# Kernel optimization log

Measured on AMD Instinct MI355X. Metric: run time of the kernel, lower is better.

The kernel has to match this reference:

```python
import jax, jax.numpy as jnp
import numpy as np

IN_FEATURES = 4096
OUT_FEATURES = 4096
BATCH = 16384


def setup_inputs() -> dict:
    key = jax.random.key(0)
    k_x, k_w, k_b = jax.random.split(key, 3)
    x = jax.random.normal(k_x, (BATCH, IN_FEATURES), dtype=jnp.float32)
    # nn.Linear default init: U(-1/sqrt(in), 1/sqrt(in))
    bound = 1.0 / np.sqrt(IN_FEATURES)
    W = jax.random.uniform(k_w, (OUT_FEATURES, IN_FEATURES), dtype=jnp.float32,
                           minval=-bound, maxval=bound)
    bias = jax.random.uniform(k_b, (OUT_FEATURES,), dtype=jnp.float32,
                              minval=-bound, maxval=bound)
    return {"x": x, "W": W, "bias": bias}


def reference(x, W, bias):
    # Algebraic reduction: sum_j (x @ W.T + b)[i, j]
    #   = x @ sum_j W[j, :] + sum_j b[j]
    weight_sums = jnp.sum(W, axis=0)          # [in_features]
    bias_sum = jnp.sum(bias)                  # scalar
    out = x @ weight_sums + bias_sum          # [batch]
    return out[:, None]                       # [batch, 1]
```

## Files before the change

### kernel.cpp

```cpp
#include <hip/hip_runtime.h>

#define IN_F 4096
#define OUT_F 4096
#define BATCH 16384

#define NCHUNK 64
#define ROWS_PER_CHUNK (OUT_F / NCHUNK)
#define PART_F4 (IN_F / 4)
#define CS_OFF   (NCHUNK * IN_F)
#define BIAS_OFF (CS_OFF + IN_F)

__global__ __launch_bounds__(256) void colsum_part(
    const float* __restrict__ W, float* __restrict__ ws) {
  int col4 = blockIdx.x * 256 + threadIdx.x;
  int row0 = blockIdx.y * ROWS_PER_CHUNK;
  const float4* W4 = (const float4*)W;

  float4 acc = make_float4(0.f, 0.f, 0.f, 0.f);
  #pragma unroll 8
  for (int r = 0; r < ROWS_PER_CHUNK; ++r) {
    float4 v = W4[(size_t)(row0 + r) * PART_F4 + col4];
    acc.x += v.x; acc.y += v.y; acc.z += v.z; acc.w += v.w;
  }
  ((float4*)ws)[(size_t)blockIdx.y * PART_F4 + col4] = acc;
}

__global__ __launch_bounds__(256) void colsum_reduce(
    const float* __restrict__ bias, float* __restrict__ ws) {
  if (blockIdx.x < 4) {
    int col4 = blockIdx.x * 256 + threadIdx.x;
    const float4* p4 = (const float4*)ws;
    float4 acc = make_float4(0.f, 0.f, 0.f, 0.f);
    #pragma unroll 8
    for (int k = 0; k < NCHUNK; ++k) {
      float4 v = p4[(size_t)k * PART_F4 + col4];
      acc.x += v.x; acc.y += v.y; acc.z += v.z; acc.w += v.w;
    }
    ((float4*)(ws + CS_OFF))[col4] = acc;
  } else if (threadIdx.x < 64) {
    float b = 0.f;
    #pragma unroll
    for (int i = 0; i < OUT_F / 64; ++i) b += bias[threadIdx.x + i * 64];
    #pragma unroll
    for (int off = 32; off > 0; off >>= 1) b += __shfl_down(b, off);
    if (threadIdx.x == 0) ws[BIAS_OFF] = b;
  }
}

__global__ __launch_bounds__(256) void rowdot_kernel(
    const float* __restrict__ x, const float* __restrict__ ws,
    float* __restrict__ out) {
  int wave = threadIdx.x >> 6;
  int lane = threadIdx.x & 63;
  int row  = blockIdx.x * 4 + wave;

  const float4* xr  = (const float4*)(x + (size_t)row * IN_F);
  const float4* cs4 = (const float4*)(ws + CS_OFF);

  float acc = 0.f;
  #pragma unroll
  for (int it = 0; it < IN_F / 4 / 64; ++it) {
    float4 xv = xr[it * 64 + lane];
    float4 wv = cs4[it * 64 + lane];
    acc += xv.x * wv.x + xv.y * wv.y + xv.z * wv.z + xv.w * wv.w;
  }
  #pragma unroll
  for (int off = 32; off > 0; off >>= 1) acc += __shfl_down(acc, off);
  if (lane == 0) out[row] = acc + ws[BIAS_OFF];
}

extern "C" void kernel_launch(void* const* d_in, const int* in_sizes, int n_in,
                              void* d_out, int out_size, void* d_ws, size_t ws_size,
                              hipStream_t stream) {
  const float* x    = (const float*)d_in[0];
  const float* W    = (const float*)d_in[1];
  const float* bias = (const float*)d_in[2];
  float* out = (float*)d_out;
  float* ws  = (float*)d_ws;

  colsum_part<<<dim3(4, NCHUNK), 256, 0, stream>>>(W, ws);
  colsum_reduce<<<5, 256, 0, stream>>>(bias, ws);
  rowdot_kernel<<<BATCH / 4, 256, 0, stream>>>(x, ws, out);
}
```

Measured before the change: 395.9 us.

## Fuse column-sum, reduce and row-dot into one cooperative persistent kernel

Replaces the three launches with a single cooperative kernel of 1024 blocks that uses grid-wide syncs between the partial column-sum, final reduction and GEMV phases. The partial column sums now use 256 chunks so the W read is spread over more blocks, and the final weight vector is staged in shared memory for the row dot products. This removes kernel launch gaps and the tail idle time of the tiny reduce kernel. In exchange it adds two grid barriers, doubles the partial-sum workspace traffic, and depends on all 1024 blocks being co-resident, with a three-kernel fallback if the cooperative launch fails.

```diff
diff --git a/kernel.cpp b/kernel.cpp
--- a/kernel.cpp
+++ b/kernel.cpp
@@ -1,42 +1,113 @@
 #include <hip/hip_runtime.h>
+#include <hip/hip_cooperative_groups.h>
+
+namespace cg = cooperative_groups;
 
 #define IN_F 4096
 #define OUT_F 4096
 #define BATCH 16384
 
-#define NCHUNK 64
+#define NBLK 1024
+#define NCHUNK 256
 #define ROWS_PER_CHUNK (OUT_F / NCHUNK)
-#define PART_F4 (IN_F / 4)
 #define CS_OFF   (NCHUNK * IN_F)
 #define BIAS_OFF (CS_OFF + IN_F)
 
+__global__ __launch_bounds__(256, 4) void fused_kernel(
+    const float* __restrict__ x, const float* __restrict__ W,
+    const float* __restrict__ bias, float* __restrict__ ws,
+    float* __restrict__ out) {
+  cg::grid_group grid = cg::this_grid();
+  const int tid = threadIdx.x;
+  const int bid = blockIdx.x;
+
+  {
+    int colgroup = bid & 3;
+    int chunk    = bid >> 2;
+    int col4     = colgroup * 256 + tid;
+    int row0     = chunk * ROWS_PER_CHUNK;
+    const float4* W4 = (const float4*)W;
+    float4 acc = make_float4(0.f, 0.f, 0.f, 0.f);
+    #pragma unroll
+    for (int r = 0; r < ROWS_PER_CHUNK; ++r) {
+      float4 v = W4[(size_t)(row0 + r) * (IN_F / 4) + col4];
+      acc.x += v.x; acc.y += v.y; acc.z += v.z; acc.w += v.w;
+    }
+    ((float4*)ws)[(size_t)chunk * (IN_F / 4) + col4] = acc;
+  }
+
+  grid.sync();
+
+  if (bid < 16) {
+    int c = bid * 256 + tid;
+    float s = 0.f;
+    #pragma unroll 8
+    for (int k = 0; k < NCHUNK; ++k) s += ws[(size_t)k * IN_F + c];
+    ws[CS_OFF + c] = s;
+  } else if (bid == 16 && tid < 64) {
+    float b = 0.f;
+    #pragma unroll
+    for (int i = 0; i < OUT_F / 64; ++i) b += bias[tid + i * 64];
+    #pragma unroll
+    for (int off = 32; off > 0; off >>= 1) b += __shfl_down(b, off);
+    if (tid == 0) ws[BIAS_OFF] = b;
+  }
+
+  grid.sync();
+
+  __shared__ float4 sw[IN_F / 4];
+  __shared__ float sbias;
+  {
+    const float4* cs4 = (const float4*)(ws + CS_OFF);
+    #pragma unroll
+    for (int i = 0; i < 4; ++i) sw[tid + i * 256] = cs4[tid + i * 256];
+    if (tid == 0) sbias = ws[BIAS_OFF];
+  }
+  __syncthreads();
+
+  int wave = tid >> 6;
+  int lane = tid & 63;
+  #pragma unroll
+  for (int r = 0; r < 4; ++r) {
+    int row = bid * 16 + r * 4 + wave;
+    const float4* xr = (const float4*)(x + (size_t)row * IN_F);
+    float acc = 0.f;
+    #pragma unroll
+    for (int it = 0; it < 16; ++it) {
+      float4 xv = xr[it * 64 + lane];
+      float4 wv = sw[it * 64 + lane];
+      acc += xv.x * wv.x + xv.y * wv.y + xv.z * wv.z + xv.w * wv.w;
+    }
+    #pragma unroll
+    for (int off = 32; off > 0; off >>= 1) acc += __shfl_down(acc, off);
+    if (lane == 0) out[row] = acc + sbias;
+  }
+}
+
 __global__ __launch_bounds__(256) void colsum_part(
     const float* __restrict__ W, float* __restrict__ ws) {
-  int col4 = blockIdx.x * 256 + threadIdx.x;
-  int row0 = blockIdx.y * ROWS_PER_CHUNK;
+  int colgroup = blockIdx.x & 3;
+  int chunk    = blockIdx.x >> 2;
+  int col4     = colgroup * 256 + threadIdx.x;
+  int row0     = chunk * ROWS_PER_CHUNK;
   const float4* W4 = (const float4*)W;
-
   float4 acc = make_float4(0.f, 0.f, 0.f, 0.f);
-  #pragma unroll 8
+  #pragma unroll
   for (int r = 0; r < ROWS_PER_CHUNK; ++r) {
-    float4 v = W4[(size_t)(row0 + r) * PART_F4 + col4];
+    float4 v = W4[(size_t)(row0 + r) * (IN_F / 4) + col4];
     acc.x += v.x; acc.y += v.y; acc.z += v.z; acc.w += v.w;
   }
-  ((float4*)ws)[(size_t)blockIdx.y * PART_F4 + col4] = acc;
+  ((float4*)ws)[(size_t)chunk * (IN_F / 4) + col4] = acc;
 }
 
 __global__ __launch_bounds__(256) void colsum_reduce(
     const float* __restrict__ bias, float* __restrict__ ws) {
-  if (blockIdx.x < 4) {
-    int col4 = blockIdx.x * 256 + threadIdx.x;
-    const float4* p4 = (const float4*)ws;
-    float4 acc = make_float4(0.f, 0.f, 0.f, 0.f);
+  if (blockIdx.x < 16) {
+    int c = blockIdx.x * 256 + threadIdx.x;
+    float s = 0.f;
     #pragma unroll 8
-    for (int k = 0; k < NCHUNK; ++k) {
-      float4 v = p4[(size_t)k * PART_F4 + col4];
-      acc.x += v.x; acc.y += v.y; acc.z += v.z; acc.w += v.w;
-    }
-    ((float4*)(ws + CS_OFF))[col4] = acc;
+    for (int k = 0; k < NCHUNK; ++k) s += ws[(size_t)k * IN_F + c];
+    ws[CS_OFF + c] = s;
   } else if (threadIdx.x < 64) {
     float b = 0.f;
     #pragma unroll
@@ -53,13 +124,11 @@
   int wave = threadIdx.x >> 6;
   int lane = threadIdx.x & 63;
   int row  = blockIdx.x * 4 + wave;
-
   const float4* xr  = (const float4*)(x + (size_t)row * IN_F);
   const float4* cs4 = (const float4*)(ws + CS_OFF);
-
   float acc = 0.f;
   #pragma unroll
-  for (int it = 0; it < IN_F / 4 / 64; ++it) {
+  for (int it = 0; it < 16; ++it) {
     float4 xv = xr[it * 64 + lane];
     float4 wv = cs4[it * 64 + lane];
     acc += xv.x * wv.x + xv.y * wv.y + xv.z * wv.z + xv.w * wv.w;
@@ -78,7 +147,13 @@
   float* out = (float*)d_out;
   float* ws  = (float*)d_ws;
 
-  colsum_part<<<dim3(4, NCHUNK), 256, 0, stream>>>(W, ws);
-  colsum_reduce<<<5, 256, 0, stream>>>(bias, ws);
-  rowdot_kernel<<<BATCH / 4, 256, 0, stream>>>(x, ws, out);
+  void* args[] = {(void*)&x, (void*)&W, (void*)&bias, (void*)&ws, (void*)&out};
+  hipError_t err = hipLaunchCooperativeKernel(
+      reinterpret_cast<void*>(fused_kernel), dim3(NBLK), dim3(256), args, 0,
+      stream);
+  if (err != hipSuccess) {
+    colsum_part<<<dim3(NBLK), 256, 0, stream>>>(W, ws);
+    colsum_reduce<<<17, 256, 0, stream>>>(bias, ws);
+    rowdot_kernel<<<BATCH / 4, 256, 0, stream>>>(x, ws, out);
+  }
 }
```

Measured after the change: 623.9 us. +57.6%, slower.
